# Performance work log

Measured on AMD Instinct MI355X. Metric: run time of the kernel, lower is better.

## Reference

```python
import jax, jax.numpy as jnp
import numpy as np

EMBED_DIM = 1024
NUM_HEADS = 16
HEAD_DIM = EMBED_DIM // NUM_HEADS


def setup_inputs() -> dict:
    key = jax.random.key(0)
    kx, kw1, kb1, kw2, kb2 = jax.random.split(key, 5)
    B, T, C = 4, 2048, EMBED_DIM
    s = 1.0 / np.sqrt(C)
    return {
        "x": jax.random.normal(kx, (B, T, C), dtype=jnp.float32),
        "qkv_w": jax.random.uniform(kw1, (3 * C, C), jnp.float32, -s, s),
        "qkv_b": jax.random.uniform(kb1, (3 * C,), jnp.float32, -s, s),
        "out_w": jax.random.uniform(kw2, (C, C), jnp.float32, -s, s),
        "out_b": jax.random.uniform(kb2, (C,), jnp.float32, -s, s),
    }


def reference(x, qkv_w, qkv_b, out_w, out_b):
    B, T, C = x.shape
    H, D = NUM_HEADS, HEAD_DIM
    qkv = x @ qkv_w.T + qkv_b                      # [B,T,3C]
    qkv = qkv.reshape(B, T, 3, H, D)
    q = qkv[:, :, 0].transpose(0, 2, 1, 3)         # [B,H,T,D]
    k = qkv[:, :, 1].transpose(0, 2, 1, 3)
    v = qkv[:, :, 2].transpose(0, 2, 1, 3)
    att = jnp.einsum("bhqd,bhkd->bhqk", q, k) / jnp.sqrt(jnp.float32(D))
    causal = jnp.tril(jnp.ones((T, T), dtype=bool))
    att = jnp.where(causal, att, -jnp.inf)
    att = jax.nn.softmax(att, axis=-1)
    out = jnp.einsum("bhqk,bhkd->bhqd", att, v)    # [B,H,T,D]
    out = out.transpose(0, 2, 1, 3).reshape(B, T, C)
    return out @ out_w.T + out_b
```

## Files before the change

### kernel.cpp

```cpp
#include <hip/hip_runtime.h>
#include <stdint.h>

typedef _Float16 f16;
typedef _Float16 f16x2 __attribute__((ext_vector_type(2)));
typedef _Float16 f16x4 __attribute__((ext_vector_type(4)));
typedef _Float16 f16x8 __attribute__((ext_vector_type(8)));
typedef float f32x4 __attribute__((ext_vector_type(4)));
typedef float f32x16 __attribute__((ext_vector_type(16)));

#define LOG2E 1.44269504088896340736f

__device__ __forceinline__ f32x4 mfma_16x16x32(f16x8 a, f16x8 b, f32x4 c) {
    return __builtin_amdgcn_mfma_f32_16x16x32_f16(a, b, c, 0, 0, 0);
}
__device__ __forceinline__ f32x16 mfma_32x32x16(f16x8 a, f16x8 b, f32x16 c) {
    return __builtin_amdgcn_mfma_f32_32x32x16_f16(a, b, c, 0, 0, 0);
}

__device__ __forceinline__ void gload_lds16(const void* g, void* l) {
    __builtin_amdgcn_global_load_lds(
        (const __attribute__((address_space(1))) unsigned int*)g,
        (__attribute__((address_space(3))) unsigned int*)l, 16, 0, 0);
}

__device__ __forceinline__ f16x2 cvt_pk_f16(float a, float b) {
    return __builtin_bit_cast(f16x2, __builtin_amdgcn_cvt_pkrtz(a, b));
}

__global__ void cast_f32_f16(const float* __restrict__ src, f16* __restrict__ dst, int n4) {
    int i = blockIdx.x * 256 + threadIdx.x;
    if (i >= n4) return;
    float4 v = reinterpret_cast<const float4*>(src)[i];
    f16x4 o;
    o[0] = (f16)v.x; o[1] = (f16)v.y; o[2] = (f16)v.z; o[3] = (f16)v.w;
    reinterpret_cast<f16x4*>(dst)[i] = o;
}

template<int MODE>
__global__ __launch_bounds__(256, 2)
void gemm_tn(const f16* __restrict__ A, const f16* __restrict__ W,
             const float* __restrict__ bias, void* __restrict__ outp,
             int M, int N, int K)
{
    __shared__ __align__(16) f16 As[128 * 32];
    __shared__ __align__(16) f16 Bs[128 * 32];

    const int lane = threadIdx.x & 63;
    const int wave = threadIdx.x >> 6;
    const int l15 = lane & 15, l4 = lane >> 4;

    const int nwg = (int)(gridDim.x * gridDim.y);
    int orig = (int)(blockIdx.y * gridDim.x + blockIdx.x);
    int cpx = nwg >> 3;
    int w = (orig & 7) * cpx + (orig >> 3);
    const int row0 = (w / (int)gridDim.x) * 128;
    const int col0 = (w % (int)gridDim.x) * 128;
    const int wr = wave >> 1, wc = wave & 1;

    f32x4 acc[4][4] = {};

    const int srow = lane >> 2;
    const int scol = (lane & 3) * 8;

    for (int k0 = 0; k0 < K; k0 += 32) {
        __syncthreads();
        #pragma unroll
        for (int it = 0; it < 2; ++it) {
            int chunk = it * 4 + wave;
            const f16* gA = A + (size_t)(row0 + chunk * 16 + srow) * K + k0 + scol;
            gload_lds16(gA, As + chunk * 512);
            const f16* gB = W + (size_t)(col0 + chunk * 16 + srow) * K + k0 + scol;
            gload_lds16(gB, Bs + chunk * 512);
        }
        __syncthreads();

        f16x8 af[4], bf[4];
        #pragma unroll
        for (int m = 0; m < 4; ++m)
            af[m] = *reinterpret_cast<const f16x8*>(As + (wr * 64 + m * 16 + l15) * 32 + l4 * 8);
        #pragma unroll
        for (int n = 0; n < 4; ++n)
            bf[n] = *reinterpret_cast<const f16x8*>(Bs + (wc * 64 + n * 16 + l15) * 32 + l4 * 8);
        #pragma unroll
        for (int m = 0; m < 4; ++m)
            #pragma unroll
            for (int n = 0; n < 4; ++n)
                acc[m][n] = mfma_16x16x32(af[m], bf[n], acc[m][n]);
    }

    if (MODE == 0) {
        f16* qb = (f16*)outp;
        const size_t HS = (size_t)64 * 2048 * 64;
        #pragma unroll
        for (int m = 0; m < 4; ++m) {
            int rbase = row0 + wr * 64 + m * 16 + l4 * 4;
            #pragma unroll
            for (int n = 0; n < 4; ++n) {
                int j = col0 + wc * 64 + n * 16 + l15;
                int which = j >> 10;
                int h = (j >> 6) & 15;
                int d = j & 63;
                float bj = bias[j];
                f16* base = qb + (size_t)which * HS;
                float scale = (which == 0) ? (0.125f * LOG2E) : 1.0f;
                #pragma unroll
                for (int r = 0; r < 4; ++r) {
                    int row = rbase + r;
                    int b = row >> 11, t = row & 2047;
                    size_t off = ((size_t)(b * 16 + h) * 2048 + t) * 64 + d;
                    base[off] = (f16)((acc[m][n][r] + bj) * scale);
                }
            }
        }
    } else {
        float* O = (float*)outp;
        #pragma unroll
        for (int m = 0; m < 4; ++m) {
            int rbase = row0 + wr * 64 + m * 16 + l4 * 4;
            #pragma unroll
            for (int n = 0; n < 4; ++n) {
                int j = col0 + wc * 64 + n * 16 + l15;
                float bj = bias[j];
                #pragma unroll
                for (int r = 0; r < 4; ++r)
                    O[(size_t)(rbase + r) * N + j] = acc[m][n][r] + bj;
            }
        }
    }
}

__global__ __launch_bounds__(256, 3)
void attn_kernel(const f16* __restrict__ qb, const f16* __restrict__ kb,
                 const f16* __restrict__ vb, f16* __restrict__ ob)
{
    __shared__ __align__(16) f16 Ks[2][4096];
    __shared__ __align__(16) f16 Vs[2][64][68];
    __shared__ __align__(16) f16 Ps[4][32][68];

    const int tid = (int)threadIdx.x;
    const int bh = (int)blockIdx.x;
    const int qblk = (int)gridDim.y - 1 - (int)blockIdx.y;
    const int lane = tid & 63;
    const int wave = tid >> 6;
    const int l31 = lane & 31;
    const int hi  = lane >> 5;
    const int q0 = qblk * 128;
    const int qw = q0 + wave * 32;

    const f16* Qp = qb + ((size_t)bh * 2048 + qw) * 64;
    f16x8 qf[4];
    #pragma unroll
    for (int ss = 0; ss < 4; ++ss)
        qf[ss] = *reinterpret_cast<const f16x8*>(Qp + l31 * 64 + ss * 16 + hi * 8);

    float Mr = -1e30f, Lr = 0.0f;
    f32x16 oacc[2] = {};

    const int ntiles = 2 * qblk + 2;
    const f16* Kbh = kb + (size_t)bh * 2048 * 64;
    const f16* Vbh = vb + (size_t)bh * 2048 * 64;

    f16x8 vld0, vld1;
    {
        #pragma unroll
        for (int it = 0; it < 2; ++it) {
            int c = it * 4 + wave;
            gload_lds16(Kbh + lane * 64 + c * 8, &Ks[0][0] + c * 512);
        }
        vld0 = *reinterpret_cast<const f16x8*>(Vbh + lane * 64 + (wave * 2 + 0) * 8);
        vld1 = *reinterpret_cast<const f16x8*>(Vbh + lane * 64 + (wave * 2 + 1) * 8);
    }

    for (int t = 0; t < ntiles; ++t) {
        const int cur = t & 1;
        const int kv0 = t * 64;

        #pragma unroll
        for (int it = 0; it < 2; ++it) {
            int dblk = wave * 2 + it;
            const f16x8 v = it ? vld1 : vld0;
            #pragma unroll
            for (int e = 0; e < 8; ++e)
                Vs[cur][dblk * 8 + e][lane] = v[e];
        }

        __syncthreads();

        {
            const int kvn = (t + 1 < ntiles) ? (t + 1) * 64 : t * 64;
            const f16* Ktn = Kbh + (size_t)kvn * 64;
            #pragma unroll
            for (int it = 0; it < 2; ++it) {
                int c = it * 4 + wave;
                gload_lds16(Ktn + lane * 64 + c * 8, &Ks[cur ^ 1][0] + c * 512);
            }
            const f16* Vtn = Vbh + (size_t)kvn * 64;
            vld0 = *reinterpret_cast<const f16x8*>(Vtn + lane * 64 + (wave * 2 + 0) * 8);
            vld1 = *reinterpret_cast<const f16x8*>(Vtn + lane * 64 + (wave * 2 + 1) * 8);
        }

        if (kv0 <= qw + 31) {
            const f16* Ksc = &Ks[cur][0];

            f32x16 s0 = {}, s1 = {};
            __builtin_amdgcn_s_setprio(1);
            #pragma unroll
            for (int ss = 0; ss < 4; ++ss) {
                f16x8 kf0 = *reinterpret_cast<const f16x8*>(Ksc + (2 * ss + hi) * 512 + l31 * 8);
                f16x8 kf1 = *reinterpret_cast<const f16x8*>(Ksc + (2 * ss + hi) * 512 + (32 + l31) * 8);
                s0 = mfma_32x32x16(kf0, qf[ss], s0);
                s1 = mfma_32x32x16(kf1, qf[ss], s1);
            }
            __builtin_amdgcn_s_setprio(0);

            if (kv0 + 63 > qw) {
                const int qg = qw + l31;
                #pragma unroll
                for (int r = 0; r < 16; ++r) {
                    int k0g = kv0 + (r & 3) + 8 * (r >> 2) + 4 * hi;
                    if (k0g > qg)      s0[r] = -1e30f;
                    if (k0g + 32 > qg) s1[r] = -1e30f;
                }
            }

            float t16[16];
            #pragma unroll
            for (int i = 0; i < 16; ++i) t16[i] = fmaxf(s0[i], s1[i]);
            #pragma unroll
            for (int st = 8; st > 0; st >>= 1)
                #pragma unroll
                for (int i = 0; i < st; ++i) t16[i] = fmaxf(t16[i], t16[i + st]);
            float mx = t16[0];
            mx = fmaxf(mx, __shfl_xor(mx, 32));

            if (__any(mx > Mr + 8.0f)) {
                float nm = fmaxf(Mr, mx);
                float alpha = exp2f(Mr - nm);
                Mr = nm; Lr *= alpha;
                float ar[16];
                #pragma unroll
                for (int r = 0; r < 16; ++r)
                    ar[r] = __shfl(alpha, (r & 3) + 8 * (r >> 2) + 4 * hi);
                #pragma unroll
                for (int r = 0; r < 16; ++r) { oacc[0][r] *= ar[r]; oacc[1][r] *= ar[r]; }
            }

            float e0[16], e1[16];
            #pragma unroll
            for (int r = 0; r < 16; ++r) {
                e0[r] = exp2f(s0[r] - Mr);
                e1[r] = exp2f(s1[r] - Mr);
            }
            float sm[16];
            #pragma unroll
            for (int i = 0; i < 16; ++i) sm[i] = e0[i] + e1[i];
            #pragma unroll
            for (int st = 8; st > 0; st >>= 1)
                #pragma unroll
                for (int i = 0; i < st; ++i) sm[i] += sm[i + st];
            float rs = sm[0];
            rs += __shfl_xor(rs, 32);
            Lr += rs;

            f16* Pw = &Ps[wave][l31][0];
            #pragma unroll
            for (int w = 0; w < 4; ++w) {
                f16x2 lo0 = cvt_pk_f16(e0[4 * w],     e0[4 * w + 1]);
                f16x2 hi0 = cvt_pk_f16(e0[4 * w + 2], e0[4 * w + 3]);
                f16x4 p4; p4[0] = lo0[0]; p4[1] = lo0[1]; p4[2] = hi0[0]; p4[3] = hi0[1];
                *reinterpret_cast<f16x4*>(Pw + 8 * w + 4 * hi) = p4;
                f16x2 lo1 = cvt_pk_f16(e1[4 * w],     e1[4 * w + 1]);
                f16x2 hi1 = cvt_pk_f16(e1[4 * w + 2], e1[4 * w + 3]);
                f16x4 q4; q4[0] = lo1[0]; q4[1] = lo1[1]; q4[2] = hi1[0]; q4[3] = hi1[1];
                *reinterpret_cast<f16x4*>(Pw + 32 + 8 * w + 4 * hi) = q4;
            }

            __builtin_amdgcn_s_setprio(1);
            #pragma unroll
            for (int ss = 0; ss < 4; ++ss) {
                f16x4 a0 = *reinterpret_cast<const f16x4*>(Pw + 16 * ss + 8 * hi);
                f16x4 a1 = *reinterpret_cast<const f16x4*>(Pw + 16 * ss + 8 * hi + 4);
                f16x8 pa = __builtin_shufflevector(a0, a1, 0, 1, 2, 3, 4, 5, 6, 7);
                #pragma unroll
                for (int db = 0; db < 2; ++db) {
                    const f16* vp = &Vs[cur][db * 32 + l31][16 * ss + 8 * hi];
                    f16x4 v0 = *reinterpret_cast<const f16x4*>(vp);
                    f16x4 v1 = *reinterpret_cast<const f16x4*>(vp + 4);
                    f16x8 vf = __builtin_shufflevector(v0, v1, 0, 1, 2, 3, 4, 5, 6, 7);
                    oacc[db] = mfma_32x32x16(pa, vf, oacc[db]);
                }
            }
            __builtin_amdgcn_s_setprio(0);
        }
    }

    float rcp = 1.0f / Lr;
    float rr[16];
    #pragma unroll
    for (int r = 0; r < 16; ++r)
        rr[r] = __shfl(rcp, (r & 3) + 8 * (r >> 2) + 4 * hi);

    const int b = bh >> 4, h = bh & 15;
    f16* O = ob + ((size_t)b * 2048 + qw) * 1024 + h * 64;
    #pragma unroll
    for (int db = 0; db < 2; ++db)
        #pragma unroll
        for (int r = 0; r < 16; ++r) {
            int q = (r & 3) + 8 * (r >> 2) + 4 * hi;
            O[(size_t)q * 1024 + db * 32 + l31] = (f16)(oacc[db][r] * rr[r]);
        }
}

extern "C" void kernel_launch(void* const* d_in, const int* in_sizes, int n_in,
                              void* d_out, int out_size, void* d_ws, size_t ws_size,
                              hipStream_t stream)
{
    const float* x    = (const float*)d_in[0];
    const float* qkvw = (const float*)d_in[1];
    const float* qkvb = (const float*)d_in[2];
    const float* outw = (const float*)d_in[3];
    const float* outb = (const float*)d_in[4];
    float* out = (float*)d_out;

    f16* x_h    = (f16*)d_ws;
    f16* qkvw_h = x_h + (size_t)8192 * 1024;
    f16* outw_h = qkvw_h + (size_t)3072 * 1024;
    f16* q_buf  = outw_h + (size_t)1024 * 1024;
    f16* att_o  = q_buf + (size_t)3 * 8388608;

    cast_f32_f16<<<8192, 256, 0, stream>>>(x, x_h, 2097152);
    cast_f32_f16<<<3072, 256, 0, stream>>>(qkvw, qkvw_h, 786432);
    cast_f32_f16<<<1024, 256, 0, stream>>>(outw, outw_h, 262144);

    gemm_tn<0><<<dim3(24, 64), 256, 0, stream>>>(x_h, qkvw_h, qkvb, q_buf, 8192, 3072, 1024);
    attn_kernel<<<dim3(64, 16), 256, 0, stream>>>(q_buf, q_buf + 8388608, q_buf + 2 * 8388608, att_o);
    gemm_tn<1><<<dim3(8, 64), 256, 0, stream>>>(att_o, outw_h, outb, out, 8192, 1024, 1024);
}
```

Before: 191.1 us.

## Double-buffer GEMM LDS tiles and pair causal query blocks in attention

The GEMM now prefetches the next K-slice into a second LDS buffer while computing the current one, which removes one barrier per iteration and overlaps loads with MFMA work. The attention kernel pairs a low and a high causal query block in each workgroup, so every workgroup does a balanced amount of work and each K/V tile load is reused by both blocks. This halves the attention grid and lowers the occupancy hint from 3 to 2 because of the extra registers and LDS. The cost is higher register pressure and fewer resident waves per CU.

```diff
diff --git a/kernel.cpp b/kernel.cpp
--- a/kernel.cpp
+++ b/kernel.cpp
@@ -42,8 +42,8 @@
              const float* __restrict__ bias, void* __restrict__ outp,
              int M, int N, int K)
 {
-    __shared__ __align__(16) f16 As[128 * 32];
-    __shared__ __align__(16) f16 Bs[128 * 32];
+    __shared__ __align__(16) f16 As[2][128 * 32];
+    __shared__ __align__(16) f16 Bs[2][128 * 32];
 
     const int lane = threadIdx.x & 63;
     const int wave = threadIdx.x >> 6;
@@ -61,31 +61,43 @@
 
     const int srow = lane >> 2;
     const int scol = (lane & 3) * 8;
-
-    for (int k0 = 0; k0 < K; k0 += 32) {
-        __syncthreads();
-        #pragma unroll
-        for (int it = 0; it < 2; ++it) {
-            int chunk = it * 4 + wave;
-            const f16* gA = A + (size_t)(row0 + chunk * 16 + srow) * K + k0 + scol;
-            gload_lds16(gA, As + chunk * 512);
-            const f16* gB = W + (size_t)(col0 + chunk * 16 + srow) * K + k0 + scol;
-            gload_lds16(gB, Bs + chunk * 512);
-        }
-        __syncthreads();
+    const int nk = K >> 5;
+
+    #pragma unroll
+    for (int it = 0; it < 2; ++it) {
+        int chunk = it * 4 + wave;
+        gload_lds16(A + (size_t)(row0 + chunk * 16 + srow) * K + scol, As[0] + chunk * 512);
+        gload_lds16(W + (size_t)(col0 + chunk * 16 + srow) * K + scol, Bs[0] + chunk * 512);
+    }
+    __syncthreads();
+
+    for (int i = 0; i < nk; ++i) {
+        const int cur = i & 1;
+
+        if (i + 1 < nk) {
+            const int k1 = (i + 1) << 5;
+            #pragma unroll
+            for (int it = 0; it < 2; ++it) {
+                int chunk = it * 4 + wave;
+                gload_lds16(A + (size_t)(row0 + chunk * 16 + srow) * K + k1 + scol, As[cur ^ 1] + chunk * 512);
+                gload_lds16(W + (size_t)(col0 + chunk * 16 + srow) * K + k1 + scol, Bs[cur ^ 1] + chunk * 512);
+            }
+        }
 
         f16x8 af[4], bf[4];
         #pragma unroll
         for (int m = 0; m < 4; ++m)
-            af[m] = *reinterpret_cast<const f16x8*>(As + (wr * 64 + m * 16 + l15) * 32 + l4 * 8);
+            af[m] = *reinterpret_cast<const f16x8*>(As[cur] + (wr * 64 + m * 16 + l15) * 32 + l4 * 8);
         #pragma unroll
         for (int n = 0; n < 4; ++n)
-            bf[n] = *reinterpret_cast<const f16x8*>(Bs + (wc * 64 + n * 16 + l15) * 32 + l4 * 8);
+            bf[n] = *reinterpret_cast<const f16x8*>(Bs[cur] + (wc * 64 + n * 16 + l15) * 32 + l4 * 8);
         #pragma unroll
         for (int m = 0; m < 4; ++m)
             #pragma unroll
             for (int n = 0; n < 4; ++n)
                 acc[m][n] = mfma_16x16x32(af[m], bf[n], acc[m][n]);
+
+        __syncthreads();
     }
 
     if (MODE == 0) {
@@ -129,34 +141,38 @@
     }
 }
 
-__global__ __launch_bounds__(256, 3)
+__global__ __launch_bounds__(256, 2)
 void attn_kernel(const f16* __restrict__ qb, const f16* __restrict__ kb,
                  const f16* __restrict__ vb, f16* __restrict__ ob)
 {
     __shared__ __align__(16) f16 Ks[2][4096];
     __shared__ __align__(16) f16 Vs[2][64][68];
-    __shared__ __align__(16) f16 Ps[4][32][68];
+    __shared__ __align__(16) f16 Ps[2][4][32][68];
 
     const int tid = (int)threadIdx.x;
     const int bh = (int)blockIdx.x;
-    const int qblk = (int)gridDim.y - 1 - (int)blockIdx.y;
+    const int p = (int)blockIdx.y;
+    const int qlo = p, qhi = 15 - p;
     const int lane = tid & 63;
     const int wave = tid >> 6;
     const int l31 = lane & 31;
     const int hi  = lane >> 5;
-    const int q0 = qblk * 128;
-    const int qw = q0 + wave * 32;
-
-    const f16* Qp = qb + ((size_t)bh * 2048 + qw) * 64;
-    f16x8 qf[4];
+
+    const int qwlo = qlo * 128 + wave * 32;
+    const int qwhi = qhi * 128 + wave * 32;
+
+    const f16* Qbh = qb + (size_t)bh * 2048 * 64;
+    f16x8 qflo[4], qfhi[4];
     #pragma unroll
-    for (int ss = 0; ss < 4; ++ss)
-        qf[ss] = *reinterpret_cast<const f16x8*>(Qp + l31 * 64 + ss * 16 + hi * 8);
-
-    float Mr = -1e30f, Lr = 0.0f;
-    f32x16 oacc[2] = {};
-
-    const int ntiles = 2 * qblk + 2;
+    for (int ss = 0; ss < 4; ++ss) {
+        qflo[ss] = *reinterpret_cast<const f16x8*>(Qbh + (size_t)(qwlo + l31) * 64 + ss * 16 + hi * 8);
+        qfhi[ss] = *reinterpret_cast<const f16x8*>(Qbh + (size_t)(qwhi + l31) * 64 + ss * 16 + hi * 8);
+    }
+
+    float Mlo = -1e30f, Llo = 0.0f, Mhi = -1e30f, Lhi = 0.0f;
+    f32x16 olo[2] = {}, ohi[2] = {};
+
+    const int ntiles = 2 * qhi + 2;
     const f16* Kbh = kb + (size_t)bh * 2048 * 64;
     const f16* Vbh = vb + (size_t)bh * 2048 * 64;
 
@@ -199,7 +215,8 @@
             vld1 = *reinterpret_cast<const f16x8*>(Vtn + lane * 64 + (wave * 2 + 1) * 8);
         }
 
-        if (kv0 <= qw + 31) {
+        auto do_group = [&](const f16x8* qf, float& Mr, float& Lr, f32x16* oacc,
+                            int qbase, int pslot) {
             const f16* Ksc = &Ks[cur][0];
 
             f32x16 s0 = {}, s1 = {};
@@ -213,8 +230,8 @@
             }
             __builtin_amdgcn_s_setprio(0);
 
-            if (kv0 + 63 > qw) {
-                const int qg = qw + l31;
+            if (kv0 + 63 > qbase) {
+                const int qg = qbase + l31;
                 #pragma unroll
                 for (int r = 0; r < 16; ++r) {
                     int k0g = kv0 + (r & 3) + 8 * (r >> 2) + 4 * hi;
@@ -262,7 +279,7 @@
             rs += __shfl_xor(rs, 32);
             Lr += rs;
 
-            f16* Pw = &Ps[wave][l31][0];
+            f16* Pw = &Ps[pslot][wave][l31][0];
             #pragma unroll
             for (int w = 0; w < 4; ++w) {
                 f16x2 lo0 = cvt_pk_f16(e0[4 * w],     e0[4 * w + 1]);
@@ -291,24 +308,43 @@
                 }
             }
             __builtin_amdgcn_s_setprio(0);
-        }
-    }
-
-    float rcp = 1.0f / Lr;
-    float rr[16];
-    #pragma unroll
-    for (int r = 0; r < 16; ++r)
-        rr[r] = __shfl(rcp, (r & 3) + 8 * (r >> 2) + 4 * hi);
+        };
+
+        if (kv0 <= qwhi + 31) do_group(qfhi, Mhi, Lhi, ohi, qwhi, 0);
+        if (kv0 <= qwlo + 31) do_group(qflo, Mlo, Llo, olo, qwlo, 1);
+    }
 
     const int b = bh >> 4, h = bh & 15;
-    f16* O = ob + ((size_t)b * 2048 + qw) * 1024 + h * 64;
-    #pragma unroll
-    for (int db = 0; db < 2; ++db)
-        #pragma unroll
-        for (int r = 0; r < 16; ++r) {
-            int q = (r & 3) + 8 * (r >> 2) + 4 * hi;
-            O[(size_t)q * 1024 + db * 32 + l31] = (f16)(oacc[db][r] * rr[r]);
-        }
+    {
+        float rcp = 1.0f / Lhi;
+        float rr[16];
+        #pragma unroll
+        for (int r = 0; r < 16; ++r)
+            rr[r] = __shfl(rcp, (r & 3) + 8 * (r >> 2) + 4 * hi);
+        f16* O = ob + ((size_t)b * 2048 + qwhi) * 1024 + h * 64;
+        #pragma unroll
+        for (int db = 0; db < 2; ++db)
+            #pragma unroll
+            for (int r = 0; r < 16; ++r) {
+                int q = (r & 3) + 8 * (r >> 2) + 4 * hi;
+                O[(size_t)q * 1024 + db * 32 + l31] = (f16)(ohi[db][r] * rr[r]);
+            }
+    }
+    {
+        float rcp = 1.0f / Llo;
+        float rr[16];
+        #pragma unroll
+        for (int r = 0; r < 16; ++r)
+            rr[r] = __shfl(rcp, (r & 3) + 8 * (r >> 2) + 4 * hi);
+        f16* O = ob + ((size_t)b * 2048 + qwlo) * 1024 + h * 64;
+        #pragma unroll
+        for (int db = 0; db < 2; ++db)
+            #pragma unroll
+            for (int r = 0; r < 16; ++r) {
+                int q = (r & 3) + 8 * (r >> 2) + 4 * hi;
+                O[(size_t)q * 1024 + db * 32 + l31] = (f16)(olo[db][r] * rr[r]);
+            }
+    }
 }
 
 extern "C" void kernel_launch(void* const* d_in, const int* in_sizes, int n_in,
@@ -333,6 +369,6 @@
     cast_f32_f16<<<1024, 256, 0, stream>>>(outw, outw_h, 262144);
 
     gemm_tn<0><<<dim3(24, 64), 256, 0, stream>>>(x_h, qkvw_h, qkvb, q_buf, 8192, 3072, 1024);
-    attn_kernel<<<dim3(64, 16), 256, 0, stream>>>(q_buf, q_buf + 8388608, q_buf + 2 * 8388608, att_o);
+    attn_kernel<<<dim3(64, 8), 256, 0, stream>>>(q_buf, q_buf + 8388608, q_buf + 2 * 8388608, att_o);
     gemm_tn<1><<<dim3(8, 64), 256, 0, stream>>>(att_o, outw_h, outb, out, 8192, 1024, 1024);
 }
```

Result: slower. 197.1 us (+3.2%).

## Double-buffer GEMM LDS tiles and pass attention P through registers via permlane swap

Applied to the files above, without the earlier changes.

The projection GEMM now double-buffers its A/W LDS tiles, prefetching the next K-slice while computing the current one, which also cuts the barriers per iteration from two to one. The attention kernel no longer round-trips the softmax probabilities through shared memory. It repacks them into the MFMA A-operand layout in registers using permlane32_swap, removing LDS writes, reads and the Ps buffer. With less LDS in use, the attention launch bound is raised to 4 blocks per CU, which raises register pressure and could cause spills.

```diff
diff --git a/kernel.cpp b/kernel.cpp
--- a/kernel.cpp
+++ b/kernel.cpp
@@ -7,6 +7,9 @@
 typedef _Float16 f16x8 __attribute__((ext_vector_type(8)));
 typedef float f32x4 __attribute__((ext_vector_type(4)));
 typedef float f32x16 __attribute__((ext_vector_type(16)));
+typedef unsigned int u32;
+typedef unsigned int u32x4 __attribute__((ext_vector_type(4)));
+typedef int i32x2 __attribute__((ext_vector_type(2)));
 
 #define LOG2E 1.44269504088896340736f
 
@@ -25,6 +28,11 @@
 
 __device__ __forceinline__ f16x2 cvt_pk_f16(float a, float b) {
     return __builtin_bit_cast(f16x2, __builtin_amdgcn_cvt_pkrtz(a, b));
+}
+
+__device__ __forceinline__ void plswap_u32(u32& a, u32& b) {
+    i32x2 r = __builtin_amdgcn_permlane32_swap((int)a, (int)b, false, false);
+    a = (u32)r[0]; b = (u32)r[1];
 }
 
 __global__ void cast_f32_f16(const float* __restrict__ src, f16* __restrict__ dst, int n4) {
@@ -42,8 +50,8 @@
              const float* __restrict__ bias, void* __restrict__ outp,
              int M, int N, int K)
 {
-    __shared__ __align__(16) f16 As[128 * 32];
-    __shared__ __align__(16) f16 Bs[128 * 32];
+    __shared__ __align__(16) f16 As[2][128 * 32];
+    __shared__ __align__(16) f16 Bs[2][128 * 32];
 
     const int lane = threadIdx.x & 63;
     const int wave = threadIdx.x >> 6;
@@ -61,31 +69,43 @@
 
     const int srow = lane >> 2;
     const int scol = (lane & 3) * 8;
-
-    for (int k0 = 0; k0 < K; k0 += 32) {
-        __syncthreads();
-        #pragma unroll
-        for (int it = 0; it < 2; ++it) {
-            int chunk = it * 4 + wave;
-            const f16* gA = A + (size_t)(row0 + chunk * 16 + srow) * K + k0 + scol;
-            gload_lds16(gA, As + chunk * 512);
-            const f16* gB = W + (size_t)(col0 + chunk * 16 + srow) * K + k0 + scol;
-            gload_lds16(gB, Bs + chunk * 512);
-        }
-        __syncthreads();
+    const int nk = K >> 5;
+
+    #pragma unroll
+    for (int it = 0; it < 2; ++it) {
+        int chunk = it * 4 + wave;
+        gload_lds16(A + (size_t)(row0 + chunk * 16 + srow) * K + scol, As[0] + chunk * 512);
+        gload_lds16(W + (size_t)(col0 + chunk * 16 + srow) * K + scol, Bs[0] + chunk * 512);
+    }
+    __syncthreads();
+
+    for (int i = 0; i < nk; ++i) {
+        const int cur = i & 1;
+
+        if (i + 1 < nk) {
+            const int k1 = (i + 1) << 5;
+            #pragma unroll
+            for (int it = 0; it < 2; ++it) {
+                int chunk = it * 4 + wave;
+                gload_lds16(A + (size_t)(row0 + chunk * 16 + srow) * K + k1 + scol, As[cur ^ 1] + chunk * 512);
+                gload_lds16(W + (size_t)(col0 + chunk * 16 + srow) * K + k1 + scol, Bs[cur ^ 1] + chunk * 512);
+            }
+        }
 
         f16x8 af[4], bf[4];
         #pragma unroll
         for (int m = 0; m < 4; ++m)
-            af[m] = *reinterpret_cast<const f16x8*>(As + (wr * 64 + m * 16 + l15) * 32 + l4 * 8);
+            af[m] = *reinterpret_cast<const f16x8*>(As[cur] + (wr * 64 + m * 16 + l15) * 32 + l4 * 8);
         #pragma unroll
         for (int n = 0; n < 4; ++n)
-            bf[n] = *reinterpret_cast<const f16x8*>(Bs + (wc * 64 + n * 16 + l15) * 32 + l4 * 8);
+            bf[n] = *reinterpret_cast<const f16x8*>(Bs[cur] + (wc * 64 + n * 16 + l15) * 32 + l4 * 8);
         #pragma unroll
         for (int m = 0; m < 4; ++m)
             #pragma unroll
             for (int n = 0; n < 4; ++n)
                 acc[m][n] = mfma_16x16x32(af[m], bf[n], acc[m][n]);
+
+        __syncthreads();
     }
 
     if (MODE == 0) {
@@ -129,13 +149,12 @@
     }
 }
 
-__global__ __launch_bounds__(256, 3)
+__global__ __launch_bounds__(256, 4)
 void attn_kernel(const f16* __restrict__ qb, const f16* __restrict__ kb,
                  const f16* __restrict__ vb, f16* __restrict__ ob)
 {
     __shared__ __align__(16) f16 Ks[2][4096];
     __shared__ __align__(16) f16 Vs[2][64][68];
-    __shared__ __align__(16) f16 Ps[4][32][68];
 
     const int tid = (int)threadIdx.x;
     const int bh = (int)blockIdx.x;
@@ -262,25 +281,25 @@
             rs += __shfl_xor(rs, 32);
             Lr += rs;
 
-            f16* Pw = &Ps[wave][l31][0];
-            #pragma unroll
-            for (int w = 0; w < 4; ++w) {
-                f16x2 lo0 = cvt_pk_f16(e0[4 * w],     e0[4 * w + 1]);
-                f16x2 hi0 = cvt_pk_f16(e0[4 * w + 2], e0[4 * w + 3]);
-                f16x4 p4; p4[0] = lo0[0]; p4[1] = lo0[1]; p4[2] = hi0[0]; p4[3] = hi0[1];
-                *reinterpret_cast<f16x4*>(Pw + 8 * w + 4 * hi) = p4;
-                f16x2 lo1 = cvt_pk_f16(e1[4 * w],     e1[4 * w + 1]);
-                f16x2 hi1 = cvt_pk_f16(e1[4 * w + 2], e1[4 * w + 3]);
-                f16x4 q4; q4[0] = lo1[0]; q4[1] = lo1[1]; q4[2] = hi1[0]; q4[3] = hi1[1];
-                *reinterpret_cast<f16x4*>(Pw + 32 + 8 * w + 4 * hi) = q4;
+            u32 cpk[2][8];
+            #pragma unroll
+            for (int B = 0; B < 4; ++B) {
+                cpk[0][2 * B]     = __builtin_bit_cast(u32, __builtin_amdgcn_cvt_pkrtz(e0[4 * B],     e0[4 * B + 1]));
+                cpk[0][2 * B + 1] = __builtin_bit_cast(u32, __builtin_amdgcn_cvt_pkrtz(e0[4 * B + 2], e0[4 * B + 3]));
+                cpk[1][2 * B]     = __builtin_bit_cast(u32, __builtin_amdgcn_cvt_pkrtz(e1[4 * B],     e1[4 * B + 1]));
+                cpk[1][2 * B + 1] = __builtin_bit_cast(u32, __builtin_amdgcn_cvt_pkrtz(e1[4 * B + 2], e1[4 * B + 3]));
             }
 
             __builtin_amdgcn_s_setprio(1);
             #pragma unroll
             for (int ss = 0; ss < 4; ++ss) {
-                f16x4 a0 = *reinterpret_cast<const f16x4*>(Pw + 16 * ss + 8 * hi);
-                f16x4 a1 = *reinterpret_cast<const f16x4*>(Pw + 16 * ss + 8 * hi + 4);
-                f16x8 pa = __builtin_shufflevector(a0, a1, 0, 1, 2, 3, 4, 5, 6, 7);
+                const int kbi = ss >> 1, qq = ss & 1;
+                u32 a0 = cpk[kbi][4 * qq + 0], b0 = cpk[kbi][4 * qq + 2];
+                u32 a1 = cpk[kbi][4 * qq + 1], b1 = cpk[kbi][4 * qq + 3];
+                plswap_u32(a0, b0);
+                plswap_u32(a1, b1);
+                u32x4 up; up[0] = a0; up[1] = a1; up[2] = b0; up[3] = b1;
+                f16x8 pa = __builtin_bit_cast(f16x8, up);
                 #pragma unroll
                 for (int db = 0; db < 2; ++db) {
                     const f16* vp = &Vs[cur][db * 32 + l31][16 * ss + 8 * hi];
```

Result: slower. 195.3 us (+2.2%).
